# Performance work log

Hardware: AMD Instinct MI355X
Metric: run time of the kernel (lower is better)

## Reference

```python
import jax, jax.numpy as jnp
import numpy as np

D_MODEL = 1024
NUM_HEADS = 16


def setup_inputs() -> dict:
    key = jax.random.key(0)
    ks = jax.random.split(key, 5)
    B, S, D = 4, 2048, D_MODEL
    scale = 0.02  # realistic init scale so logits stay well-conditioned
    return {
        "x": jax.random.normal(ks[0], (B, S, D), dtype=jnp.float32),
        "Wq": jax.random.normal(ks[1], (D, D), dtype=jnp.float32) * scale,
        "Wk": jax.random.normal(ks[2], (D, D), dtype=jnp.float32) * scale,
        "Wv": jax.random.normal(ks[3], (D, D), dtype=jnp.float32) * scale,
        "Wo": jax.random.normal(ks[4], (D, D), dtype=jnp.float32) * scale,
    }


def reference(x, Wq, Wk, Wv, Wo):
    # x: (B, S, D). Weights are (d_out, d_in) as in the torch module.
    B, S, D = x.shape
    H = NUM_HEADS
    dk = D // H

    # Projections: einsum('oi,bli->blo') == x @ W.T
    q = jnp.einsum("oi,bsi->bso", Wq, x).reshape(B, S, H, dk).transpose(0, 2, 1, 3)
    k = jnp.einsum("oi,bsi->bso", Wk, x).reshape(B, S, H, dk).transpose(0, 2, 1, 3)
    v = jnp.einsum("oi,bsi->bso", Wv, x).reshape(B, S, H, dk).transpose(0, 2, 1, 3)

    # Scaled dot-product scores per head: (B, H, S, S)
    scores = jnp.einsum("bhqd,bhkd->bhqk", q, k) / jnp.sqrt(jnp.asarray(dk, x.dtype))

    # Causal mask (True = keep); masked entries get -inf (matches inf-subtraction)
    causal = jnp.tril(jnp.ones((S, S), dtype=bool))
    scores = jnp.where(causal, scores, -jnp.inf)

    attn = jax.nn.softmax(scores, axis=-1)

    out = jnp.einsum("bhqk,bhkd->bhqd", attn, v)  # (B, H, S, dk)
    out = out.transpose(0, 2, 1, 3).reshape(B, S, D)  # concat heads

    # Output projection: einsum('oi,bli->blo')
    return jnp.einsum("oi,bsi->bso", Wo, out)
```

## Files before the change

kernel.cpp:

```cpp
#include <hip/hip_runtime.h>
#include <hip/hip_bf16.h>

typedef unsigned short u16;
typedef __attribute__((ext_vector_type(8))) short short8;
typedef __attribute__((ext_vector_type(4))) float f32x4;

#if __has_builtin(__builtin_amdgcn_exp2f)
#define EXP2F(x) __builtin_amdgcn_exp2f(x)
#else
#define EXP2F(x) exp2f(x)
#endif

__device__ __forceinline__ float bf2f(u16 v) {
    union { unsigned u; float f; } c; c.u = ((unsigned)v) << 16; return c.f;
}
__device__ __forceinline__ u16 f2bf(float f) {
    union { float f; unsigned u; } c; c.f = f;
    unsigned r = c.u + 0x7fffu + ((c.u >> 16) & 1u);
    return (u16)(r >> 16);
}
__device__ __forceinline__ uint4 pack8(const float4 a, const float4 b) {
    uint4 r;
    r.x = (unsigned)f2bf(a.x) | ((unsigned)f2bf(a.y) << 16);
    r.y = (unsigned)f2bf(a.z) | ((unsigned)f2bf(a.w) << 16);
    r.z = (unsigned)f2bf(b.x) | ((unsigned)f2bf(b.y) << 16);
    r.w = (unsigned)f2bf(b.z) | ((unsigned)f2bf(b.w) << 16);
    return r;
}
__device__ __forceinline__ void gl_lds16(const u16* g, u16* l) {
    __builtin_amdgcn_global_load_lds((const __attribute__((address_space(1))) unsigned int*)g,
                                     (__attribute__((address_space(3))) unsigned int*)l, 16, 0, 0);
}

__global__ __launch_bounds__(256) void convert_all(const float* __restrict__ x,
                                                   const float* __restrict__ wq,
                                                   const float* __restrict__ wk,
                                                   const float* __restrict__ wv,
                                                   const float* __restrict__ wo,
                                                   u16* xb, u16* wqb, u16* wkb, u16* wvb, u16* wob) {
    size_t i8 = ((size_t)blockIdx.x * 256 + threadIdx.x) * 8;
    const float* src; u16* dst; size_t off;
    if (i8 < 8388608) { src = x; dst = xb; off = i8; }
    else {
        size_t idx = i8 - 8388608;
        int w = (int)(idx >> 20); off = idx & 1048575;
        src = (w == 0) ? wq : (w == 1) ? wk : (w == 2) ? wv : wo;
        dst = (w == 0) ? wqb : (w == 1) ? wkb : (w == 2) ? wvb : wob;
    }
    float4 a = *(const float4*)&src[off];
    float4 b = *(const float4*)&src[off + 4];
    *(uint4*)&dst[off] = pack8(a, b);
}

__device__ __forceinline__ void core_dual(const u16* __restrict__ A,
                                          const u16* __restrict__ B0,
                                          const u16* __restrict__ B1,
                                          int m0, int n0a, int n0b,
                                          u16* As, u16* Bs0, u16* Bs1,
                                          f32x4 acc0[2][4], f32x4 acc1[2][4]) {
    const int tid = threadIdx.x;
    const int wid = tid >> 6, lane = tid & 63, lr = lane & 15, quad = lane >> 4;
    const int srow = lane >> 3;
    const int scg  = (lane & 7) ^ srow;
    const int wm = (wid >> 1) * 32, wn = (wid & 1) * 64;
    const int r0 = wid * 16;

    for (int kt = 0; kt < 1024; kt += 64) {
        __syncthreads();
        #pragma unroll
        for (int h = 0; h < 2; ++h) {
            int r = r0 + h * 8;
            gl_lds16(&A [(size_t)(m0  + r + srow) * 1024 + kt + scg * 8], &As [r * 64]);
            gl_lds16(&B0[(size_t)(n0a + r + srow) * 1024 + kt + scg * 8], &Bs0[r * 64]);
            gl_lds16(&B1[(size_t)(n0b + r + srow) * 1024 + kt + scg * 8], &Bs1[r * 64]);
        }
        __syncthreads();
        #pragma unroll
        for (int c = 0; c < 2; ++c) {
            short8 af[2], bf[4];
            #pragma unroll
            for (int mi = 0; mi < 2; ++mi)
                af[mi] = *(const short8*)&As[(wm + mi * 16 + lr) * 64 + (((c * 4 + quad) ^ (lr & 7)) * 8)];
            #pragma unroll
            for (int ni = 0; ni < 4; ++ni)
                bf[ni] = *(const short8*)&Bs0[(wn + ni * 16 + lr) * 64 + (((c * 4 + quad) ^ (lr & 7)) * 8)];
            #pragma unroll
            for (int mi = 0; mi < 2; ++mi)
                #pragma unroll
                for (int ni = 0; ni < 4; ++ni)
                    acc0[mi][ni] = __builtin_amdgcn_mfma_f32_16x16x32_bf16(af[mi], bf[ni], acc0[mi][ni], 0, 0, 0);
            #pragma unroll
            for (int ni = 0; ni < 4; ++ni)
                bf[ni] = *(const short8*)&Bs1[(wn + ni * 16 + lr) * 64 + (((c * 4 + quad) ^ (lr & 7)) * 8)];
            #pragma unroll
            for (int mi = 0; mi < 2; ++mi)
                #pragma unroll
                for (int ni = 0; ni < 4; ++ni)
                    acc1[mi][ni] = __builtin_amdgcn_mfma_f32_16x16x32_bf16(af[mi], bf[ni], acc1[mi][ni], 0, 0, 0);
        }
    }
}

__global__ __launch_bounds__(512, 4) void gemm_qkv(const u16* __restrict__ xb,
                                                   const u16* __restrict__ wq,
                                                   const u16* __restrict__ wk,
                                                   const u16* __restrict__ wv,
                                                   u16* __restrict__ Qb, u16* __restrict__ Kb,
                                                   u16* __restrict__ Vtb) {
    __shared__ __align__(16) u16 As [8192];
    __shared__ __align__(16) u16 Bs0[8192];
    __shared__ __align__(16) u16 Bs1[8192];
    const int bid = blockIdx.x;

    f32x4 acc0[2][4], acc1[2][4];
    #pragma unroll
    for (int a = 0; a < 2; ++a)
        #pragma unroll
        for (int b = 0; b < 4; ++b) { acc0[a][b] = 0; acc1[a][b] = 0; }

    const int lane = threadIdx.x & 63, lr = lane & 15, quad = lane >> 4;
    const int wid = threadIdx.x >> 6;
    const int wm = (wid >> 1) * 32, wn = (wid & 1) * 64;

    if (bid < 512) {
        const int xcd = bid & 7;
        const int i   = bid >> 3;
        const int m0  = (xcd * 8 + (i & 7)) * 128;
        const int n0  = (i >> 3) * 128;
        core_dual(xb, wq, wk, m0, n0, n0, As, Bs0, Bs1, acc0, acc1);
        #pragma unroll
        for (int mi = 0; mi < 2; ++mi)
            #pragma unroll
            for (int ni = 0; ni < 4; ++ni)
                #pragma unroll
                for (int reg = 0; reg < 4; ++reg) {
                    int row = m0 + wm + mi * 16 + quad * 4 + reg;
                    int col = n0 + wn + ni * 16 + lr;
                    int bhh = (row >> 11) * 16 + (col >> 6);
                    size_t o = (size_t)bhh * 131072 + (size_t)(row & 2047) * 64 + (col & 63);
                    Qb[o] = f2bf(acc0[mi][ni][reg] * 0.18033688f);
                    Kb[o] = f2bf(acc1[mi][ni][reg]);
                }
    } else {
        const int t   = bid - 512;
        const int xcd = t & 7;
        const int j   = t >> 3;
        const int m0  = (j & 7) * 128;
        const int np  = xcd * 4 + (j >> 3);
        const int n0a = np * 256, n0b = np * 256 + 128;
        core_dual(wv, xb, xb, m0, n0a, n0b, As, Bs0, Bs1, acc0, acc1);
        #pragma unroll
        for (int half = 0; half < 2; ++half) {
            const int nb = half ? n0b : n0a;
            #pragma unroll
            for (int mi = 0; mi < 2; ++mi)
                #pragma unroll
                for (int ni = 0; ni < 4; ++ni)
                    #pragma unroll
                    for (int reg = 0; reg < 4; ++reg) {
                        int row = m0 + wm + mi * 16 + quad * 4 + reg;
                        int col = nb + wn + ni * 16 + lr;
                        int bhh = (col >> 11) * 16 + (row >> 6);
                        float v = half ? acc1[mi][ni][reg] : acc0[mi][ni][reg];
                        Vtb[(size_t)bhh * 131072 + (size_t)(row & 63) * 2048 + (col & 2047)] = f2bf(v);
                    }
        }
    }
}

__global__ __launch_bounds__(512, 4) void gemm_out(const u16* __restrict__ Ob,
                                                   const u16* __restrict__ wo,
                                                   float* __restrict__ C) {
    __shared__ __align__(16) u16 As [8192];
    __shared__ __align__(16) u16 Bs0[8192];
    __shared__ __align__(16) u16 Bs1[8192];
    const int bid = blockIdx.x;
    const int xcd = bid & 7;
    const int i   = bid >> 3;
    const int m0  = (xcd * 8 + (i & 7)) * 128;
    const int np  = i >> 3;
    const int n0a = np * 256, n0b = np * 256 + 128;

    f32x4 acc0[2][4], acc1[2][4];
    #pragma unroll
    for (int a = 0; a < 2; ++a)
        #pragma unroll
        for (int b = 0; b < 4; ++b) { acc0[a][b] = 0; acc1[a][b] = 0; }

    core_dual(Ob, wo, wo, m0, n0a, n0b, As, Bs0, Bs1, acc0, acc1);

    const int lane = threadIdx.x & 63, lr = lane & 15, quad = lane >> 4;
    const int wid = threadIdx.x >> 6;
    const int wm = (wid >> 1) * 32, wn = (wid & 1) * 64;
    #pragma unroll
    for (int mi = 0; mi < 2; ++mi)
        #pragma unroll
        for (int ni = 0; ni < 4; ++ni)
            #pragma unroll
            for (int reg = 0; reg < 4; ++reg) {
                int row = m0 + wm + mi * 16 + quad * 4 + reg;
                int col = wn + ni * 16 + lr;
                C[(size_t)row * 1024 + n0a + col] = acc0[mi][ni][reg];
                C[(size_t)row * 1024 + n0b + col] = acc1[mi][ni][reg];
            }
}

__global__ __launch_bounds__(512, 4) void attn_flash(const u16* __restrict__ Q,
                                                     const u16* __restrict__ K,
                                                     const u16* __restrict__ Vt,
                                                     u16* __restrict__ O) {
    __shared__ __align__(16) u16 Kbuf[2][4096];
    __shared__ __align__(16) u16 Vbuf[2][4096];
    __shared__ __align__(16) u16 Ps[8][2048];

    const int tid = threadIdx.x, wave = tid >> 6, lane = tid & 63;
    const int lr = lane & 15, quad = lane >> 4;
    const int bh = blockIdx.x & 63;
    const int p  = blockIdx.x >> 6;
    const int qt8 = (p < 4) ? (7 - p) : (p - 4);
    const int qbase = qt8 * 256 + wave * 32;
    const size_t base = (size_t)bh * 131072;

    const int srow = lane >> 3;
    const int scg  = (lane & 7) ^ srow;

    const short8 onesv = {0x3f80, 0x3f80, 0x3f80, 0x3f80, 0x3f80, 0x3f80, 0x3f80, 0x3f80};

    short8 qf[2][2];
    #pragma unroll
    for (int qmi = 0; qmi < 2; ++qmi)
        #pragma unroll
        for (int c = 0; c < 2; ++c)
            qf[qmi][c] = *(const short8*)&Q[base + (size_t)(qbase + qmi * 16 + lr) * 64 + c * 32 + quad * 8];

    f32x4 oacc[4][2];
    #pragma unroll
    for (int i = 0; i < 4; ++i) { oacc[i][0] = 0; oacc[i][1] = 0; }
    f32x4 lacc[2];
    lacc[0] = 0; lacc[1] = 0;

    const int jmax = 4 * qt8 + 3;
    const int r0 = wave * 8;

    gl_lds16(&K[base + (size_t)(r0 + srow) * 64 + scg * 8], &Kbuf[0][r0 * 64]);
    gl_lds16(&Vt[base + (size_t)(r0 + srow) * 2048 + scg * 8], &Vbuf[0][r0 * 64]);

    for (int j = 0; j <= jmax; ++j) {
        const int buf = j & 1;
        __syncthreads();
        if (j < jmax) {
            const int nb = buf ^ 1;
            gl_lds16(&K[base + (size_t)((j + 1) * 64 + r0 + srow) * 64 + scg * 8], &Kbuf[nb][r0 * 64]);
            gl_lds16(&Vt[base + (size_t)(r0 + srow) * 2048 + (j + 1) * 64 + scg * 8], &Vbuf[nb][r0 * 64]);
        }

        if (j * 64 <= qbase + 31) {
            f32x4 st[4][2];
            #pragma unroll
            for (int ni = 0; ni < 4; ++ni) { st[ni][0] = 0; st[ni][1] = 0; }
            __builtin_amdgcn_s_setprio(1);
            #pragma unroll
            for (int c = 0; c < 2; ++c) {
                short8 kf[4];
                #pragma unroll
                for (int ni = 0; ni < 4; ++ni)
                    kf[ni] = *(const short8*)&Kbuf[buf][(ni * 16 + lr) * 64 + (((c * 4 + quad) ^ (lr & 7)) * 8)];
                #pragma unroll
                for (int ni = 0; ni < 4; ++ni)
                    #pragma unroll
                    for (int qmi = 0; qmi < 2; ++qmi)
                        st[ni][qmi] = __builtin_amdgcn_mfma_f32_16x16x32_bf16(kf[ni], qf[qmi][c], st[ni][qmi], 0, 0, 0);
            }
            __builtin_amdgcn_s_setprio(0);

            if (j >= 4 * qt8) {
                #pragma unroll
                for (int ni = 0; ni < 4; ++ni)
                    #pragma unroll
                    for (int qmi = 0; qmi < 2; ++qmi)
                        #pragma unroll
                        for (int reg = 0; reg < 4; ++reg) {
                            int key = j * 64 + ni * 16 + quad * 4 + reg;
                            int q   = qbase + qmi * 16 + lr;
                            if (key > q) st[ni][qmi][reg] = -3.0e38f;
                        }
            }

            #pragma unroll
            for (int qmi = 0; qmi < 2; ++qmi) {
                #pragma unroll
                for (int ni = 0; ni < 4; ++ni) {
                    unsigned u0 = __float_as_uint(EXP2F(st[ni][qmi][0]));
                    unsigned u1 = __float_as_uint(EXP2F(st[ni][qmi][1]));
                    unsigned u2 = __float_as_uint(EXP2F(st[ni][qmi][2]));
                    unsigned u3 = __float_as_uint(EXP2F(st[ni][qmi][3]));
                    uint2 pk;
                    pk.x = __builtin_amdgcn_perm(u1, u0, 0x07060302);
                    pk.y = __builtin_amdgcn_perm(u3, u2, 0x07060302);
                    int g8 = ni * 2 + (quad >> 1);
                    *(uint2*)&Ps[wave][qmi * 1024 + lr * 64 + ((g8 ^ (lr & 7)) * 8 + (quad & 1) * 4)] = pk;
                }
            }

            __builtin_amdgcn_s_setprio(1);
            #pragma unroll
            for (int c = 0; c < 2; ++c) {
                short8 pf[2];
                #pragma unroll
                for (int qmi = 0; qmi < 2; ++qmi)
                    pf[qmi] = *(const short8*)&Ps[wave][qmi * 1024 + lr * 64 + (((c * 4 + quad) ^ (lr & 7)) * 8)];
                #pragma unroll
                for (int dmi = 0; dmi < 4; ++dmi) {
                    short8 vf = *(const short8*)&Vbuf[buf][(dmi * 16 + lr) * 64 + (((c * 4 + quad) ^ (lr & 7)) * 8)];
                    #pragma unroll
                    for (int qmi = 0; qmi < 2; ++qmi)
                        oacc[dmi][qmi] = __builtin_amdgcn_mfma_f32_16x16x32_bf16(vf, pf[qmi], oacc[dmi][qmi], 0, 0, 0);
                }
                #pragma unroll
                for (int qmi = 0; qmi < 2; ++qmi)
                    lacc[qmi] = __builtin_amdgcn_mfma_f32_16x16x32_bf16(onesv, pf[qmi], lacc[qmi], 0, 0, 0);
            }
            __builtin_amdgcn_s_setprio(0);
        }
    }

    const int b = bh >> 4, h = bh & 15;
    #pragma unroll
    for (int qmi = 0; qmi < 2; ++qmi) {
        float rl = 1.0f / lacc[qmi][0];
        int s = qbase + qmi * 16 + lr;
        #pragma unroll
        for (int dmi = 0; dmi < 4; ++dmi) {
            unsigned o0 = f2bf(oacc[dmi][qmi][0] * rl);
            unsigned o1 = f2bf(oacc[dmi][qmi][1] * rl);
            unsigned o2 = f2bf(oacc[dmi][qmi][2] * rl);
            unsigned o3 = f2bf(oacc[dmi][qmi][3] * rl);
            uint2 pk;
            pk.x = o0 | (o1 << 16);
            pk.y = o2 | (o3 << 16);
            *(uint2*)&O[((size_t)(b * 2048 + s)) * 1024 + h * 64 + dmi * 16 + quad * 4] = pk;
        }
    }
}

extern "C" void kernel_launch(void* const* d_in, const int* in_sizes, int n_in,
                              void* d_out, int out_size, void* d_ws, size_t ws_size,
                              hipStream_t stream) {
    const float* x  = (const float*)d_in[0];
    const float* Wq = (const float*)d_in[1];
    const float* Wk = (const float*)d_in[2];
    const float* Wv = (const float*)d_in[3];
    const float* Wo = (const float*)d_in[4];

    u16* xb  = (u16*)d_ws;
    u16* wqb = xb + 8388608;
    u16* wkb = wqb + 1048576;
    u16* wvb = wkb + 1048576;
    u16* wob = wvb + 1048576;
    u16* Qb  = wob + 1048576;
    u16* Kb  = Qb + 8388608;
    u16* Vtb = Kb + 8388608;
    u16* Ob  = xb;

    convert_all<<<6144, 256, 0, stream>>>(x, Wq, Wk, Wv, Wo, xb, wqb, wkb, wvb, wob);

    gemm_qkv<<<768, 512, 0, stream>>>(xb, wqb, wkb, wvb, Qb, Kb, Vtb);

    attn_flash<<<512, 512, 0, stream>>>(Qb, Kb, Vtb, Ob);

    gemm_out<<<256, 512, 0, stream>>>(Ob, wob, (float*)d_out);
}
```

Baseline: 231.0 us.

## Halve attention block size to 4 waves with 128-row query tiles

```diff
diff --git a/kernel.cpp b/kernel.cpp
--- a/kernel.cpp
+++ b/kernel.cpp
@@ -205,20 +205,20 @@
             }
 }
 
-__global__ __launch_bounds__(512, 4) void attn_flash(const u16* __restrict__ Q,
+__global__ __launch_bounds__(256, 4) void attn_flash(const u16* __restrict__ Q,
                                                      const u16* __restrict__ K,
                                                      const u16* __restrict__ Vt,
                                                      u16* __restrict__ O) {
     __shared__ __align__(16) u16 Kbuf[2][4096];
     __shared__ __align__(16) u16 Vbuf[2][4096];
-    __shared__ __align__(16) u16 Ps[8][2048];
+    __shared__ __align__(16) u16 Ps[4][1024];
 
     const int tid = threadIdx.x, wave = tid >> 6, lane = tid & 63;
     const int lr = lane & 15, quad = lane >> 4;
     const int bh = blockIdx.x & 63;
     const int p  = blockIdx.x >> 6;
-    const int qt8 = (p < 4) ? (7 - p) : (p - 4);
-    const int qbase = qt8 * 256 + wave * 32;
+    const int qt = (p < 8) ? (15 - p) : (p - 8);
+    const int qbase = qt * 128 + wave * 32;
     const size_t base = (size_t)bh * 131072;
 
     const int srow = lane >> 3;
@@ -239,19 +239,27 @@
     f32x4 lacc[2];
     lacc[0] = 0; lacc[1] = 0;
 
-    const int jmax = 4 * qt8 + 3;
-    const int r0 = wave * 8;
-
-    gl_lds16(&K[base + (size_t)(r0 + srow) * 64 + scg * 8], &Kbuf[0][r0 * 64]);
-    gl_lds16(&Vt[base + (size_t)(r0 + srow) * 2048 + scg * 8], &Vbuf[0][r0 * 64]);
+    const int jmax = 2 * qt + 1;
+    const int r0 = wave * 16;
+
+    #pragma unroll
+    for (int h = 0; h < 2; ++h) {
+        int r = r0 + h * 8;
+        gl_lds16(&K[base + (size_t)(r + srow) * 64 + scg * 8], &Kbuf[0][r * 64]);
+        gl_lds16(&Vt[base + (size_t)(r + srow) * 2048 + scg * 8], &Vbuf[0][r * 64]);
+    }
 
     for (int j = 0; j <= jmax; ++j) {
         const int buf = j & 1;
         __syncthreads();
         if (j < jmax) {
             const int nb = buf ^ 1;
-            gl_lds16(&K[base + (size_t)((j + 1) * 64 + r0 + srow) * 64 + scg * 8], &Kbuf[nb][r0 * 64]);
-            gl_lds16(&Vt[base + (size_t)(r0 + srow) * 2048 + (j + 1) * 64 + scg * 8], &Vbuf[nb][r0 * 64]);
+            #pragma unroll
+            for (int h = 0; h < 2; ++h) {
+                int r = r0 + h * 8;
+                gl_lds16(&K[base + (size_t)((j + 1) * 64 + r + srow) * 64 + scg * 8], &Kbuf[nb][r * 64]);
+                gl_lds16(&Vt[base + (size_t)(r + srow) * 2048 + (j + 1) * 64 + scg * 8], &Vbuf[nb][r * 64]);
+            }
         }
 
         if (j * 64 <= qbase + 31) {
@@ -273,7 +281,7 @@
             }
             __builtin_amdgcn_s_setprio(0);
 
-            if (j >= 4 * qt8) {
+            if (j >= 2 * qt) {
                 #pragma unroll
                 for (int ni = 0; ni < 4; ++ni)
                     #pragma unroll
@@ -298,29 +306,21 @@
                     pk.x = __builtin_amdgcn_perm(u1, u0, 0x07060302);
                     pk.y = __builtin_amdgcn_perm(u3, u2, 0x07060302);
                     int g8 = ni * 2 + (quad >> 1);
-                    *(uint2*)&Ps[wave][qmi * 1024 + lr * 64 + ((g8 ^ (lr & 7)) * 8 + (quad & 1) * 4)] = pk;
+                    *(uint2*)&Ps[wave][lr * 64 + ((g8 ^ (lr & 7)) * 8 + (quad & 1) * 4)] = pk;
                 }
-            }
-
-            __builtin_amdgcn_s_setprio(1);
-            #pragma unroll
-            for (int c = 0; c < 2; ++c) {
-                short8 pf[2];
-                #pragma unroll
-                for (int qmi = 0; qmi < 2; ++qmi)
-                    pf[qmi] = *(const short8*)&Ps[wave][qmi * 1024 + lr * 64 + (((c * 4 + quad) ^ (lr & 7)) * 8)];
-                #pragma unroll
-                for (int dmi = 0; dmi < 4; ++dmi) {
-                    short8 vf = *(const short8*)&Vbuf[buf][(dmi * 16 + lr) * 64 + (((c * 4 + quad) ^ (lr & 7)) * 8)];
+                __builtin_amdgcn_s_setprio(1);
+                #pragma unroll
+                for (int c = 0; c < 2; ++c) {
+                    short8 pf = *(const short8*)&Ps[wave][lr * 64 + (((c * 4 + quad) ^ (lr & 7)) * 8)];
                     #pragma unroll
-                    for (int qmi = 0; qmi < 2; ++qmi)
-                        oacc[dmi][qmi] = __builtin_amdgcn_mfma_f32_16x16x32_bf16(vf, pf[qmi], oacc[dmi][qmi], 0, 0, 0);
+                    for (int dmi = 0; dmi < 4; ++dmi) {
+                        short8 vf = *(const short8*)&Vbuf[buf][(dmi * 16 + lr) * 64 + (((c * 4 + quad) ^ (lr & 7)) * 8)];
+                        oacc[dmi][qmi] = __builtin_amdgcn_mfma_f32_16x16x32_bf16(vf, pf, oacc[dmi][qmi], 0, 0, 0);
+                    }
+                    lacc[qmi] = __builtin_amdgcn_mfma_f32_16x16x32_bf16(onesv, pf, lacc[qmi], 0, 0, 0);
                 }
-                #pragma unroll
-                for (int qmi = 0; qmi < 2; ++qmi)
-                    lacc[qmi] = __builtin_amdgcn_mfma_f32_16x16x32_bf16(onesv, pf[qmi], lacc[qmi], 0, 0, 0);
-            }
-            __builtin_amdgcn_s_setprio(0);
+                __builtin_amdgcn_s_setprio(0);
+            }
         }
     }
 
@@ -366,7 +366,7 @@
 
     gemm_qkv<<<768, 512, 0, stream>>>(xb, wqb, wkb, wvb, Qb, Kb, Vtb);
 
-    attn_flash<<<512, 512, 0, stream>>>(Qb, Kb, Vtb, Ob);
+    attn_flash<<<1024, 256, 0, stream>>>(Qb, Kb, Vtb, Ob);
 
     gemm_out<<<256, 512, 0, stream>>>(Ob, wob, (float*)d_out);
 }
```

New measurement: 234.9 us. No clear change (+1.7%).
